# Kernel optimization log

Hardware: AMD Instinct MI355X
Metric: run time of the kernel (lower is better)

Reference implementation:

```python
import jax, jax.numpy as jnp
import numpy as np

BN_EPS = 1e-5

# Fixed shifted-difference kernels from the torch module (4,1,3,3)
_W1 = np.array([[[-1, 0, 0], [0, 1, 0], [0, 0, 0]],
                [[0, -1, 0], [0, 1, 0], [0, 0, 0]],
                [[0, 0, -1], [0, 1, 0], [0, 0, 0]],
                [[0, 0, 0], [-1, 1, 0], [0, 0, 0]]], dtype=np.float32).reshape(4, 1, 3, 3)
_W2 = np.ascontiguousarray(_W1[:, :, ::-1, ::-1])
SHIFTS = (1, 3)


def _conv(x, w, dilation=1):
    return jax.lax.conv_general_dilated(
        x, w, window_strides=(1, 1), padding='SAME',
        rhs_dilation=(dilation, dilation),
        dimension_numbers=('NCHW', 'OIHW', 'NCHW'))


def setup_inputs() -> dict:
    key = jax.random.key(0)
    ks = jax.random.split(key, 3)
    B, C, H, W = 4, 32, 512, 512
    cen = jax.random.normal(ks[0], (B, C, H, W), dtype=jnp.float32)
    w_conv = jax.random.normal(ks[1], (C, C, 3, 3), dtype=jnp.float32) * (1.0 / np.sqrt(9 * C))
    w_1x1 = jax.random.normal(ks[2], (1, C, 1, 1), dtype=jnp.float32) * (1.0 / np.sqrt(C))
    return {
        'cen': cen,
        'w_conv': w_conv,
        'bn_gamma': jnp.ones((C,), jnp.float32),
        'bn_beta': jnp.zeros((C,), jnp.float32),
        'bn_mean': jnp.zeros((C,), jnp.float32),
        'bn_var': jnp.ones((C,), jnp.float32),
        'w_1x1': w_1x1,
        'b_1x1': jnp.zeros((1,), jnp.float32),
    }


def reference(cen, w_conv, bn_gamma, bn_beta, bn_mean, bn_var, w_1x1, b_1x1):
    k1 = jnp.asarray(_W1)
    k2 = jnp.asarray(_W2)

    # down_conv: BaseConv(C->C, k3, s1) = Conv(no bias) + BN(eval) + SiLU, then 1x1 conv C->1
    x = _conv(cen, w_conv)
    inv = bn_gamma / jnp.sqrt(bn_var + BN_EPS)
    x = x * inv[None, :, None, None] + (bn_beta - bn_mean * inv)[None, :, None, None]
    x = jax.nn.silu(x)
    x = _conv(x, w_1x1) + b_1x1[None, :, None, None]  # [B,1,H,W]

    # circ_shift per dilation: fixed diff convs, product, min over 4 directions
    outs = []
    for s in SHIFTS:
        o1 = _conv(x, k1, dilation=s)  # [B,4,H,W]
        o2 = _conv(x, k2, dilation=s)
        outs.append(jnp.min(o1 * o2, axis=1, keepdims=True))  # [B,1,H,W]
    outs = jnp.stack(outs, axis=-1)  # [B,1,H,W,n_shifts]

    att = (jnp.max(outs, axis=-1) + jnp.mean(outs, axis=-1)) * 0.5
    att = jax.nn.sigmoid(jax.nn.relu(att))  # [B,1,H,W]
    return cen * att
```

## Files before the change

### kernel.cpp

```cpp
#include <hip/hip_runtime.h>
#include <hip/hip_bf16.h>
#include <math.h>

typedef __attribute__((ext_vector_type(8))) short bf16x8;
typedef __attribute__((ext_vector_type(4))) float f32x4;

#define HH 512
#define WW 512
#define CC 32

__device__ __forceinline__ unsigned short f2bf(float f) {
    unsigned u = __float_as_uint(f);
    u = (u + 0x7fffu + ((u >> 16) & 1u)) >> 16;
    return (unsigned short)u;
}

__global__ __launch_bounds__(256) void prepack(const float* __restrict__ wconv,
                                               unsigned short* __restrict__ wbuf) {
    int e = blockIdx.x * 256 + threadIdx.x;
    if (e < 9216) {
        int co  = e / 288;
        int rem = e - co * 288;
        int ci  = rem / 9;
        int t   = rem - ci * 9;
        wbuf[((t * 4 + (ci >> 3)) * 32 + co) * 8 + (ci & 7)] = f2bf(wconv[e]);
    }
}

__global__ __launch_bounds__(256) void conv_fused(
    const float* __restrict__ cen, const unsigned short* __restrict__ wbuf,
    const float* __restrict__ gamma, const float* __restrict__ beta,
    const float* __restrict__ mean, const float* __restrict__ var,
    const float* __restrict__ w1x1, const float* __restrict__ b1x1,
    float* __restrict__ xout)
{
    __shared__ unsigned short sIn[18 * 34 * 32];

    const int tid = threadIdx.x;
    const int b  = blockIdx.z;
    const int i0 = blockIdx.y << 4;
    const int j0 = blockIdx.x << 5;

    for (int e = tid; e < 16 * 612; e += 256) {
        int cp = e & 15;
        int sp = ((e >> 6) << 2) | ((e >> 4) & 3);
        int y = sp / 34, x = sp - y * 34;
        int gy = i0 - 1 + y, gx = j0 - 1 + x;
        float v0 = 0.f, v1 = 0.f;
        if ((unsigned)gy < HH && (unsigned)gx < WW) {
            const float* p = cen + (((long)(b * CC + 2 * cp) * HH + gy) * WW + gx);
            v0 = p[0];
            v1 = p[(long)HH * WW];
        }
        unsigned pk = (unsigned)f2bf(v0) | ((unsigned)f2bf(v1) << 16);
        int off = sp * 32 + ((((cp >> 2) ^ (sp & 3)) << 3) | ((cp & 3) << 1));
        *(unsigned*)&sIn[off] = pk;
    }

    const int lane = tid & 63;
    const int wv   = tid >> 6;
    const int l15  = lane & 15;
    const int h    = lane >> 4;

    bf16x8 Bf[9][2];
#pragma unroll
    for (int t = 0; t < 9; ++t)
#pragma unroll
        for (int n = 0; n < 2; ++n)
            Bf[t][n] = *(const bf16x8*)&wbuf[((t * 4 + h) * 32 + n * 16 + l15) * 8];

    const float iv0 = gamma[l15]      / sqrtf(var[l15]      + 1e-5f);
    const float iv1 = gamma[l15 + 16] / sqrtf(var[l15 + 16] + 1e-5f);
    const float bb0 = beta[l15]      - mean[l15]      * iv0;
    const float bb1 = beta[l15 + 16] - mean[l15 + 16] * iv1;
    const float wa0 = w1x1[l15], wa1 = w1x1[l15 + 16];
    const float bias = b1x1[0];

    __syncthreads();

#pragma unroll
    for (int mt = 0; mt < 8; ++mt) {
        const int iloc = wv * 4 + (mt >> 1);
        const int jg   = mt & 1;
        const int xb   = jg * 16 + l15;
        f32x4 acc0 = {0.f, 0.f, 0.f, 0.f};
        f32x4 acc1 = {0.f, 0.f, 0.f, 0.f};
#pragma unroll
        for (int t = 0; t < 9; ++t) {
            const int sp = (iloc + t / 3) * 34 + xb + t % 3;
            bf16x8 A = *(const bf16x8*)&sIn[sp * 32 + ((h ^ (sp & 3)) << 3)];
            acc0 = __builtin_amdgcn_mfma_f32_16x16x32_bf16(A, Bf[t][0], acc0, 0, 0, 0);
            acc1 = __builtin_amdgcn_mfma_f32_16x16x32_bf16(A, Bf[t][1], acc1, 0, 0, 0);
        }
        float v[4];
#pragma unroll
        for (int r = 0; r < 4; ++r) {
            float y0 = acc0[r] * iv0 + bb0;
            float y1 = acc1[r] * iv1 + bb1;
            float s0 = y0 / (1.f + __expf(-y0));
            float s1 = y1 / (1.f + __expf(-y1));
            v[r] = wa0 * s0 + wa1 * s1;
        }
#pragma unroll
        for (int m = 1; m <= 8; m <<= 1) {
#pragma unroll
            for (int r = 0; r < 4; ++r)
                v[r] += __shfl_xor(v[r], m, 64);
        }
        if (l15 == 0) {
            const int i = i0 + iloc;
            const int j = j0 + jg * 16 + 4 * h;
            f32x4 o = {v[0] + bias, v[1] + bias, v[2] + bias, v[3] + bias};
            *(f32x4*)&xout[((long)b * HH + i) * WW + j] = o;
        }
    }
}

__device__ __forceinline__ float ldx(const float* __restrict__ xp, int i, int j) {
    return ((unsigned)i < HH && (unsigned)j < WW) ? xp[i * WW + j] : 0.f;
}

__global__ __launch_bounds__(256) void att_mul(
    const float* __restrict__ xin, const float* __restrict__ cen,
    float* __restrict__ out)
{
    const int t  = blockIdx.x * 256 + threadIdx.x;
    const int j4 = t & 127;
    const int i  = (t >> 7) & 511;
    const int b  = t >> 16;
    const float* xp = xin + (long)b * HH * WW;
    const int j = j4 << 2;

    float att[4];
#pragma unroll
    for (int p = 0; p < 4; ++p) {
        const int jj = j + p;
        const float c = xp[i * WW + jj];
        float o[2];
#pragma unroll
        for (int si = 0; si < 2; ++si) {
            const int s = si ? 3 : 1;
            float um = ldx(xp, i - s, jj - s), uc = ldx(xp, i - s, jj), up = ldx(xp, i - s, jj + s);
            float lm = ldx(xp, i,     jj - s),                          rp = ldx(xp, i,     jj + s);
            float dm = ldx(xp, i + s, jj - s), dc = ldx(xp, i + s, jj), dp = ldx(xp, i + s, jj + s);
            float d0 = (c - um) * (c - dp);
            float d1 = (c - uc) * (c - dc);
            float d2 = (c - up) * (c - dm);
            float d3 = (c - lm) * (c - rp);
            o[si] = fminf(fminf(d0, d1), fminf(d2, d3));
        }
        float a = 0.5f * (fmaxf(o[0], o[1]) + 0.5f * (o[0] + o[1]));
        a = a > 0.f ? a : 0.f;
        att[p] = 1.f / (1.f + __expf(-a));
    }

    const long rowoff = ((long)b * CC * HH + i) * WW + j;
#pragma unroll 8
    for (int c = 0; c < CC; ++c) {
        const long off = rowoff + (long)c * HH * WW;
        f32x4 v = *(const f32x4*)&cen[off];
        v.x *= att[0]; v.y *= att[1]; v.z *= att[2]; v.w *= att[3];
        *(f32x4*)&out[off] = v;
    }
}

extern "C" void kernel_launch(void* const* d_in, const int* in_sizes, int n_in,
                              void* d_out, int out_size, void* d_ws, size_t ws_size,
                              hipStream_t stream) {
    const float* cen   = (const float*)d_in[0];
    const float* wconv = (const float*)d_in[1];
    const float* gamma = (const float*)d_in[2];
    const float* beta  = (const float*)d_in[3];
    const float* mean  = (const float*)d_in[4];
    const float* var   = (const float*)d_in[5];
    const float* w1x1  = (const float*)d_in[6];
    const float* b1x1  = (const float*)d_in[7];
    float* xbuf = (float*)d_ws;
    unsigned short* wbuf = (unsigned short*)((char*)d_ws + (4l << 20));
    float* outp = (float*)d_out;

    prepack<<<dim3(36), 256, 0, stream>>>(wconv, wbuf);
    conv_fused<<<dim3(16, 32, 4), 256, 0, stream>>>(
        cen, wbuf, gamma, beta, mean, var, w1x1, b1x1, xbuf);
    att_mul<<<dim3(1024), 256, 0, stream>>>(xbuf, cen, outp);
}
```

Baseline: 357.5 us.

## Vectorize conv halo loads and stage att stencil rows in shared memory

New measurement: 316.4 us. -11.5%, faster.

```diff
diff --git a/kernel.cpp b/kernel.cpp
--- a/kernel.cpp
+++ b/kernel.cpp
@@ -34,27 +34,34 @@
     const float* __restrict__ w1x1, const float* __restrict__ b1x1,
     float* __restrict__ xout)
 {
-    __shared__ unsigned short sIn[18 * 34 * 32];
+    __shared__ unsigned short sIn[18 * 40 * 32];
 
     const int tid = threadIdx.x;
     const int b  = blockIdx.z;
     const int i0 = blockIdx.y << 4;
     const int j0 = blockIdx.x << 5;
 
-    for (int e = tid; e < 16 * 612; e += 256) {
-        int cp = e & 15;
-        int sp = ((e >> 6) << 2) | ((e >> 4) & 3);
-        int y = sp / 34, x = sp - y * 34;
-        int gy = i0 - 1 + y, gx = j0 - 1 + x;
-        float v0 = 0.f, v1 = 0.f;
-        if ((unsigned)gy < HH && (unsigned)gx < WW) {
-            const float* p = cen + (((long)(b * CC + 2 * cp) * HH + gy) * WW + gx);
-            v0 = p[0];
-            v1 = p[(long)HH * WW];
-        }
-        unsigned pk = (unsigned)f2bf(v0) | ((unsigned)f2bf(v1) << 16);
-        int off = sp * 32 + ((((cp >> 2) ^ (sp & 3)) << 3) | ((cp & 3) << 1));
-        *(unsigned*)&sIn[off] = pk;
+    for (int e = tid; e < 2880; e += 256) {
+        int r   = e / 160;
+        int rem = e - r * 160;
+        int cp  = rem & 15;
+        int q   = rem >> 4;
+        int gy  = i0 - 1 + r;
+        int gx0 = j0 - 4 + 4 * q;
+        f32x4 v0 = {0.f, 0.f, 0.f, 0.f}, v1 = {0.f, 0.f, 0.f, 0.f};
+        if ((unsigned)gy < HH && (unsigned)gx0 < (WW - 3)) {
+            const float* p = cen + (((long)(b * CC + 2 * cp) * HH + gy) * WW + gx0);
+            v0 = *(const f32x4*)p;
+            v1 = *(const f32x4*)(p + (long)HH * WW);
+        }
+        const int spb = r * 40 + 4 * q;
+#pragma unroll
+        for (int p2 = 0; p2 < 4; ++p2) {
+            int sp = spb + p2;
+            unsigned pk = (unsigned)f2bf(v0[p2]) | ((unsigned)f2bf(v1[p2]) << 16);
+            int off = sp * 32 + ((((cp >> 2) ^ (sp & 3)) << 3) | ((cp & 3) << 1));
+            *(unsigned*)&sIn[off] = pk;
+        }
     }
 
     const int lane = tid & 63;
@@ -87,7 +94,7 @@
         f32x4 acc1 = {0.f, 0.f, 0.f, 0.f};
 #pragma unroll
         for (int t = 0; t < 9; ++t) {
-            const int sp = (iloc + t / 3) * 34 + xb + t % 3;
+            const int sp = (iloc + t / 3) * 40 + xb + t % 3 + 3;
             bf16x8 A = *(const bf16x8*)&sIn[sp * 32 + ((h ^ (sp & 3)) << 3)];
             acc0 = __builtin_amdgcn_mfma_f32_16x16x32_bf16(A, Bf[t][0], acc0, 0, 0, 0);
             acc1 = __builtin_amdgcn_mfma_f32_16x16x32_bf16(A, Bf[t][1], acc1, 0, 0, 0);
@@ -116,40 +123,65 @@
     }
 }
 
-__device__ __forceinline__ float ldx(const float* __restrict__ xp, int i, int j) {
-    return ((unsigned)i < HH && (unsigned)j < WW) ? xp[i * WW + j] : 0.f;
-}
-
 __global__ __launch_bounds__(256) void att_mul(
     const float* __restrict__ xin, const float* __restrict__ cen,
     float* __restrict__ out)
 {
-    const int t  = blockIdx.x * 256 + threadIdx.x;
-    const int j4 = t & 127;
-    const int i  = (t >> 7) & 511;
-    const int b  = t >> 16;
+    __shared__ float xs[8 * 520];
+    const int tid = threadIdx.x;
+    const int b   = blockIdx.x >> 8;
+    const int ip  = blockIdx.x & 255;
+    const int gy0 = 2 * ip - 3;
     const float* xp = xin + (long)b * HH * WW;
-    const int j = j4 << 2;
+
+    for (int e = tid; e < 1040; e += 256) {
+        int r  = e / 130;
+        int q  = e - r * 130;
+        int gy = gy0 + r;
+        int gx0 = 4 * q - 4;
+        f32x4 v = {0.f, 0.f, 0.f, 0.f};
+        if ((unsigned)gy < HH && (unsigned)gx0 < (WW - 3))
+            v = *(const f32x4*)&xp[gy * WW + gx0];
+        *(f32x4*)&xs[r * 520 + 4 * q] = v;
+    }
+    __syncthreads();
+
+    const int jq = tid & 127;
+    const int il = tid >> 7;
+    const int i  = 2 * ip + il;
+    const int j  = jq << 2;
+
+    float w3m[12], w1m[12], wc0[12], w1p[12], w3p[12];
+#pragma unroll
+    for (int k = 0; k < 3; ++k) {
+        f32x4 a;
+        a = *(const f32x4*)&xs[(il + 0) * 520 + 4 * (jq + k)];
+        w3m[4*k] = a.x; w3m[4*k+1] = a.y; w3m[4*k+2] = a.z; w3m[4*k+3] = a.w;
+        a = *(const f32x4*)&xs[(il + 2) * 520 + 4 * (jq + k)];
+        w1m[4*k] = a.x; w1m[4*k+1] = a.y; w1m[4*k+2] = a.z; w1m[4*k+3] = a.w;
+        a = *(const f32x4*)&xs[(il + 3) * 520 + 4 * (jq + k)];
+        wc0[4*k] = a.x; wc0[4*k+1] = a.y; wc0[4*k+2] = a.z; wc0[4*k+3] = a.w;
+        a = *(const f32x4*)&xs[(il + 4) * 520 + 4 * (jq + k)];
+        w1p[4*k] = a.x; w1p[4*k+1] = a.y; w1p[4*k+2] = a.z; w1p[4*k+3] = a.w;
+        a = *(const f32x4*)&xs[(il + 6) * 520 + 4 * (jq + k)];
+        w3p[4*k] = a.x; w3p[4*k+1] = a.y; w3p[4*k+2] = a.z; w3p[4*k+3] = a.w;
+    }
 
     float att[4];
 #pragma unroll
     for (int p = 0; p < 4; ++p) {
-        const int jj = j + p;
-        const float c = xp[i * WW + jj];
-        float o[2];
-#pragma unroll
-        for (int si = 0; si < 2; ++si) {
-            const int s = si ? 3 : 1;
-            float um = ldx(xp, i - s, jj - s), uc = ldx(xp, i - s, jj), up = ldx(xp, i - s, jj + s);
-            float lm = ldx(xp, i,     jj - s),                          rp = ldx(xp, i,     jj + s);
-            float dm = ldx(xp, i + s, jj - s), dc = ldx(xp, i + s, jj), dp = ldx(xp, i + s, jj + s);
-            float d0 = (c - um) * (c - dp);
-            float d1 = (c - uc) * (c - dc);
-            float d2 = (c - up) * (c - dm);
-            float d3 = (c - lm) * (c - rp);
-            o[si] = fminf(fminf(d0, d1), fminf(d2, d3));
-        }
-        float a = 0.5f * (fmaxf(o[0], o[1]) + 0.5f * (o[0] + o[1]));
+        const float c = wc0[p + 4];
+        float d0 = (c - w1m[p + 3]) * (c - w1p[p + 5]);
+        float d1 = (c - w1m[p + 4]) * (c - w1p[p + 4]);
+        float d2 = (c - w1m[p + 5]) * (c - w1p[p + 3]);
+        float d3 = (c - wc0[p + 3]) * (c - wc0[p + 5]);
+        float o0 = fminf(fminf(d0, d1), fminf(d2, d3));
+        d0 = (c - w3m[p + 1]) * (c - w3p[p + 7]);
+        d1 = (c - w3m[p + 4]) * (c - w3p[p + 4]);
+        d2 = (c - w3m[p + 7]) * (c - w3p[p + 1]);
+        d3 = (c - wc0[p + 1]) * (c - wc0[p + 7]);
+        float o1 = fminf(fminf(d0, d1), fminf(d2, d3));
+        float a = 0.5f * (fmaxf(o0, o1) + 0.5f * (o0 + o1));
         a = a > 0.f ? a : 0.f;
         att[p] = 1.f / (1.f + __expf(-a));
     }
```
